# Optimization experiments

Hardware: AMD Instinct MI355X
Metric: run time of the kernel (lower is better)

The kernel has to match this reference:

```python
import jax, jax.numpy as jnp
import numpy as np

N = 50000      # nodes
E = 800000     # edges
H = 8          # heads
D = 16         # per-head dim (hidden_channels)
HD = H * D     # 128
G = 64         # graphs in batch
BN_EPS = 1e-5


def setup_inputs() -> dict:
    key = jax.random.key(0)
    ks = iter(jax.random.split(key, 40))
    s = lambda *shape: jax.random.normal(next(ks), shape, dtype=jnp.float32) * 0.05
    inp = {
        "X": jax.random.normal(next(ks), (N, 1), dtype=jnp.float32),
        "edge_index": jax.random.randint(next(ks), (2, E), 0, N, dtype=jnp.int32),
        "batch": jnp.sort(jax.random.randint(next(ks), (N,), 0, G, dtype=jnp.int32)),
        # layer 1: in=1 -> H*D
        "Wq1": s(1, HD), "bq1": jnp.zeros((HD,), jnp.float32),
        "Wk1": s(1, HD), "bk1": jnp.zeros((HD,), jnp.float32),
        "Wv1": s(1, HD), "bv1": jnp.zeros((HD,), jnp.float32),
        "Ws1": s(1, HD), "bs1": jnp.zeros((HD,), jnp.float32),
        # layers 2-5 stacked: in=HD -> H*D
        "Wq": s(4, HD, HD), "bq": jnp.zeros((4, HD), jnp.float32),
        "Wk": s(4, HD, HD), "bk": jnp.zeros((4, HD), jnp.float32),
        "Wv": s(4, HD, HD), "bv": jnp.zeros((4, HD), jnp.float32),
        "Ws": s(4, HD, HD), "bs": jnp.zeros((4, HD), jnp.float32),
        # batchnorms (5 of them)
        "bn_gamma": jnp.ones((5, HD), jnp.float32),
        "bn_beta": jnp.zeros((5, HD), jnp.float32),
        "Wr": s(HD, 1), "br": jnp.zeros((1,), jnp.float32),
    }
    return inp


def _transformer_conv(x, src, dst, Wq, bq, Wk, bk, Wv, bv, Ws, bs):
    """PyG TransformerConv (concat=True, root_weight=True, beta=False), eval mode."""
    n = x.shape[0]
    q = (x @ Wq + bq).reshape(n, H, D)
    k = (x @ Wk + bk).reshape(n, H, D)
    v = (x @ Wv + bv).reshape(n, H, D)
    # per-edge attention logits: query at destination, key at source
    alpha = jnp.sum(q[dst] * k[src], axis=-1) / jnp.sqrt(jnp.float32(D))  # [E,H]
    # segment softmax over incoming edges of each destination node
    amax = jax.ops.segment_max(alpha, dst, num_segments=n)                # [N,H]
    amax = jnp.where(jnp.isfinite(amax), amax, 0.0)
    ex = jnp.exp(alpha - amax[dst])
    denom = jax.ops.segment_sum(ex, dst, num_segments=n) + 1e-16         # [N,H]
    w = ex / denom[dst]                                                  # [E,H]
    out = jax.ops.segment_sum(v[src] * w[:, :, None], dst, num_segments=n)  # [N,H,D]
    return out.reshape(n, HD) + (x @ Ws + bs)                            # root skip


def _bn(x, gamma, beta):
    mu = jnp.mean(x, axis=0)
    var = jnp.mean(jnp.square(x - mu), axis=0)  # biased, as torch BN training
    return (x - mu) * jax.lax.rsqrt(var + BN_EPS) * gamma + beta


def reference(X, edge_index, batch, Wq1, bq1, Wk1, bk1, Wv1, bv1, Ws1, bs1,
              Wq, bq, Wk, bk, Wv, bv, Ws, bs, bn_gamma, bn_beta, Wr, br):
    src, dst = edge_index[0], edge_index[1]
    x = jax.nn.relu(_transformer_conv(X, src, dst, Wq1, bq1, Wk1, bk1, Wv1, bv1, Ws1, bs1))
    x = _bn(x, bn_gamma[0], bn_beta[0])
    for i in range(4):  # layers 2..5 with residuals (dropout = identity in eval)
        h = jax.nn.relu(_transformer_conv(x, src, dst, Wq[i], bq[i], Wk[i], bk[i],
                                          Wv[i], bv[i], Ws[i], bs[i]))
        x = _bn(h, bn_gamma[i + 1], bn_beta[i + 1]) + x
    # global mean pool over graphs
    sums = jax.ops.segment_sum(x, batch, num_segments=G, indices_are_sorted=True)
    cnts = jax.ops.segment_sum(jnp.ones((x.shape[0],), x.dtype), batch,
                               num_segments=G, indices_are_sorted=True)
    x_mean = sums / jnp.maximum(cnts, 1.0)[:, None]
    pred = x_mean @ Wr + br
    return pred, x_mean
```

## Files before the change

kernel.cpp:

```cpp
#include <hip/hip_runtime.h>
#include <hip/hip_fp16.h>
#include <math.h>

#define HD 128
#define NGRAPH 64

typedef _Float16 f16x8 __attribute__((ext_vector_type(8)));
typedef _Float16 f16x2 __attribute__((ext_vector_type(2)));
typedef float    f32x4 __attribute__((ext_vector_type(4)));

__device__ __forceinline__ unsigned h2bits(__half2 h){ return *(unsigned*)&h; }

__device__ __forceinline__ float fdot2u(unsigned a, unsigned b, float c){
#if __has_builtin(__builtin_amdgcn_fdot2)
  return __builtin_amdgcn_fdot2(*(f16x2*)&a, *(f16x2*)&b, c, false);
#else
  float2 fa = __half22float2(*(__half2*)&a);
  float2 fb = __half22float2(*(__half2*)&b);
  return c + fa.x*fb.x + fa.y*fb.y;
#endif
}

__global__ __launch_bounds__(256) void k_count_setup(
    const int* __restrict__ dst, int* __restrict__ deg, int* __restrict__ epos, int E, int EB,
    const float* __restrict__ X,
    const float* __restrict__ Wq1, const float* __restrict__ bq1,
    const float* __restrict__ Wk1, const float* __restrict__ bk1,
    const float* __restrict__ Wv1, const float* __restrict__ bv1,
    const float* __restrict__ Ws1, const float* __restrict__ bs1,
    const float* __restrict__ Wq, const float* __restrict__ Wk,
    const float* __restrict__ Wv, const float* __restrict__ Ws,
    const int* __restrict__ batch, int* __restrict__ gstart,
    uint4* __restrict__ Wpack,
    unsigned* __restrict__ qh_u, unsigned* __restrict__ kvh_u, unsigned* __restrict__ h_u,
    int N, int L1B){
  int b = blockIdx.x;
  int tid = threadIdx.x;
  if (b < EB){
    int e = b*256 + tid;
    if (e < E) epos[e] = atomicAdd(&deg[dst[e]], 1);
  } else if (b < EB + L1B){
    int idx = (b - EB)*256 + tid;
    if (idx >= N*32) return;
    int n = idx >> 5, s4 = idx & 31, c = s4 << 2;
    float xv = X[n];
    float qv[4], kk[4], vv[4], hv[4];
    #pragma unroll
    for (int i = 0; i < 4; ++i){
      qv[i] = xv*Wq1[c+i] + bq1[c+i];
      kk[i] = xv*Wk1[c+i] + bk1[c+i];
      vv[i] = xv*Wv1[c+i] + bv1[c+i];
      hv[i] = xv*Ws1[c+i] + bs1[c+i];
    }
    uint2 hw;
    hw.x = h2bits(__floats2half2_rn(hv[0], hv[1]));
    hw.y = h2bits(__floats2half2_rn(hv[2], hv[3]));
    *(uint2*)&h_u[(size_t)n*64 + (c >> 1)] = hw;
    uint2 qw;
    qw.x = h2bits(__floats2half2_rn(qv[0], qv[1]));
    qw.y = h2bits(__floats2half2_rn(qv[2], qv[3]));
    *(uint2*)&qh_u[(size_t)n*64 + (c >> 1)] = qw;
    int head = c >> 4, ch = c & 15;
    size_t kbase = (size_t)n*128 + head*16 + (ch >> 1);
    uint2 kw, vw;
    kw.x = h2bits(__floats2half2_rn(kk[0], kk[1]));
    kw.y = h2bits(__floats2half2_rn(kk[2], kk[3]));
    vw.x = h2bits(__floats2half2_rn(vv[0], vv[1]));
    vw.y = h2bits(__floats2half2_rn(vv[2], vv[3]));
    *(uint2*)&kvh_u[kbase]     = kw;
    *(uint2*)&kvh_u[kbase + 8] = vw;
  } else if (b < EB + L1B + 128){
    int idx = (b - EB - L1B)*256 + tid;
    int mi   = idx >> 11;
    int rem  = idx & 2047;
    int lane = rem & 63;
    int tile = rem >> 6;
    int chunk = tile >> 3, nt = tile & 7;
    int l = mi >> 2, ws = mi & 3;
    const float* W = (ws==0?Wq:ws==1?Wk:ws==2?Wv:Ws) + (size_t)l*HD*HD;
    int quad = lane >> 4;
    int n = nt*16 + (lane & 15);
    int k0 = chunk*32 + quad*8;
    __half hs[8];
    #pragma unroll
    for (int j = 0; j < 8; ++j) hs[j] = __float2half(W[(size_t)(k0+j)*HD + n]);
    Wpack[idx] = *(uint4*)hs;
  } else {
    int g = tid;
    if (g > NGRAPH) return;
    int lo = 0, hi = N;
    while (lo < hi){
      int mid = (lo + hi) >> 1;
      if (batch[mid] < g) lo = mid + 1; else hi = mid;
    }
    gstart[g] = lo;
  }
}

__global__ __launch_bounds__(256) void k_scan1(const int* __restrict__ deg, int* __restrict__ rp,
                                               int* __restrict__ bt, int N){
  __shared__ int sm[256];
  int i = blockIdx.x*256 + threadIdx.x;
  int v = (i < N) ? deg[i] : 0;
  sm[threadIdx.x] = v;
  __syncthreads();
  for (int off = 1; off < 256; off <<= 1){
    int t = (threadIdx.x >= (unsigned)off) ? sm[threadIdx.x - off] : 0;
    __syncthreads();
    sm[threadIdx.x] += t;
    __syncthreads();
  }
  if (i < N) rp[i+1] = sm[threadIdx.x];
  if (threadIdx.x == 255) bt[blockIdx.x] = sm[255];
  if (blockIdx.x == 0 && threadIdx.x == 0) rp[0] = 0;
}

__global__ __launch_bounds__(256) void k_scan3(int* __restrict__ rp, const int* __restrict__ bt, int N){
  __shared__ int sm[256];
  int b = blockIdx.x, t = threadIdx.x;
  sm[t] = (t < b) ? bt[t] : 0;
  __syncthreads();
  for (int off = 128; off > 0; off >>= 1){
    if (t < off) sm[t] += sm[t + off];
    __syncthreads();
  }
  int offset = sm[0];
  int i = b*256 + t;
  if (i < N) rp[i+1] += offset;
}

__global__ __launch_bounds__(256) void k_scatter(const int* __restrict__ src, const int* __restrict__ dst,
                                                 const int* __restrict__ rp, const int* __restrict__ epos,
                                                 int* __restrict__ srcs, int E){
  int e = blockIdx.x*256 + threadIdx.x;
  if (e < E) srcs[rp[dst[e]] + epos[e]] = src[e];
}

__global__ __launch_bounds__(256) void k_gemm(
    const __half* __restrict__ x, const uint4* __restrict__ Wpack,
    const float* __restrict__ bq, const float* __restrict__ bk,
    const float* __restrict__ bv, const float* __restrict__ bs,
    unsigned* __restrict__ qh_u, unsigned* __restrict__ kvh_u, unsigned* __restrict__ h_u,
    int N, int layer){
  __shared__ uint4 Bs[2048];
  int wsel = blockIdx.y;
  const uint4* Wm = Wpack + (size_t)(layer*4 + wsel)*2048;
  int tid = threadIdx.x;
  for (int i = tid; i < 2048; i += 256) Bs[i] = Wm[i];

  int w = tid >> 6, lane = tid & 63;
  int l15 = lane & 15, quad = lane >> 4;
  const float* bias = (wsel==0)?bq:(wsel==1)?bk:(wsel==2)?bv:bs;

  __syncthreads();

  for (int rt = 0; rt < 4; ++rt){
    int row0 = blockIdx.x*256 + w*64 + rt*16;
    if (row0 >= N) break;
    int arow = row0 + l15;

    f32x4 acc[8];
    #pragma unroll
    for (int i = 0; i < 8; ++i) acc[i] = (f32x4){0.f,0.f,0.f,0.f};

    #pragma unroll
    for (int chunk = 0; chunk < 4; ++chunk){
      f16x8 a = {};
      if (arow < N) a = *(const f16x8*)(x + (size_t)arow*HD + chunk*32 + quad*8);
      #pragma unroll
      for (int nt = 0; nt < 8; ++nt){
        f16x8 b = *(const f16x8*)&Bs[(chunk*8 + nt)*64 + lane];
        acc[nt] = __builtin_amdgcn_mfma_f32_16x16x32_f16(a, b, acc[nt], 0, 0, 0);
      }
    }

    #pragma unroll
    for (int nt = 0; nt < 8; ++nt){
      int col = nt*16 + l15;
      float b = bias[col];
      #pragma unroll
      for (int reg = 0; reg < 4; ++reg){
        float val = acc[nt][reg] + b;
        float oth = __shfl_xor(val, 1);
        int row = row0 + quad*4 + reg;
        if (!(l15 & 1) && row < N){
          unsigned pk = h2bits(__floats2half2_rn(val, oth));
          if (wsel == 0)       qh_u[(size_t)row*64  + nt*8  + (l15>>1)]      = pk;
          else if (wsel == 1)  kvh_u[(size_t)row*128 + nt*16 + (l15>>1)]     = pk;
          else if (wsel == 2)  kvh_u[(size_t)row*128 + nt*16 + (l15>>1) + 8] = pk;
          else                 h_u[(size_t)row*64  + nt*8  + (l15>>1)]       = pk;
        }
      }
    }
  }
}

__global__ __launch_bounds__(256) void k_attn(
    const uint4* __restrict__ qh4, const uint4* __restrict__ kvh4,
    unsigned* __restrict__ h_u, float* __restrict__ pr2,
    const int* __restrict__ rp, const int* __restrict__ srcs, int N, int layer){
  __shared__ float ssum[4][128];
  __shared__ float ssq[4][128];
  int tid = threadIdx.x;
  int w = tid >> 6, lane = tid & 63;
  int oct = lane >> 3, hh = lane & 7;
  int n = blockIdx.x*4 + w;
  bool active = (n < N);

  float acc[16];
  #pragma unroll
  for (int i = 0; i < 16; ++i) acc[i] = 0.f;
  float lsum = 0.f;

  if (active){
    uint4 q0 = qh4[(size_t)n*16 + hh*2];
    uint4 q1 = qh4[(size_t)n*16 + hh*2 + 1];
    unsigned qr[8] = {q0.x,q0.y,q0.z,q0.w, q1.x,q1.y,q1.z,q1.w};
    int beg = rp[n], end = rp[n+1];
    int t = beg + oct;
    bool vcur = (t < end);
    uint4 g0, g1, g2, g3;
    if (vcur){
      const uint4* base = kvh4 + (size_t)srcs[t]*32 + hh*4;
      g0 = base[0]; g1 = base[1]; g2 = base[2]; g3 = base[3];
    }
    while (vcur){
      int tn = t + 8;
      bool vn = (tn < end);
      int sn = vn ? srcs[tn] : 0;
      const uint4* nb = kvh4 + (size_t)sn*32 + hh*4;
      uint4 n0 = nb[0], n1 = nb[1], n2 = nb[2], n3 = nb[3];

      unsigned kr[8] = {g0.x,g0.y,g0.z,g0.w, g1.x,g1.y,g1.z,g1.w};
      float pd = 0.f;
      #pragma unroll
      for (int i = 0; i < 8; ++i) pd = fdot2u(kr[i], qr[i], pd);
      float e = __expf(pd * 0.25f);
      lsum += e;
      unsigned vr[8] = {g2.x,g2.y,g2.z,g2.w, g3.x,g3.y,g3.z,g3.w};
      #pragma unroll
      for (int i = 0; i < 8; ++i){
        float2 vf = __half22float2(*(__half2*)&vr[i]);
        acc[2*i]   += e*vf.x;
        acc[2*i+1] += e*vf.y;
      }
      g0 = n0; g1 = n1; g2 = n2; g3 = n3;
      t = tn; vcur = vn;
    }
  }

  #pragma unroll
  for (int mask = 8; mask <= 32; mask <<= 1){
    lsum += __shfl_xor(lsum, mask);
    #pragma unroll
    for (int i = 0; i < 16; ++i) acc[i] += __shfl_xor(acc[i], mask);
  }
  float inv = (lsum > 0.f) ? 1.f/lsum : 0.f;

  float out[16];
  #pragma unroll
  for (int i = 0; i < 16; ++i) out[i] = 0.f;
  if (active && oct == 0){
    uint4* hp = (uint4*)(h_u + (size_t)n*64 + hh*8);
    uint4 s0 = hp[0], s1 = hp[1];
    unsigned sr[8] = {s0.x,s0.y,s0.z,s0.w, s1.x,s1.y,s1.z,s1.w};
    #pragma unroll
    for (int i = 0; i < 8; ++i){
      float2 sk = __half22float2(*(__half2*)&sr[i]);
      out[2*i]   = fmaxf(acc[2*i]*inv   + sk.x, 0.f);
      out[2*i+1] = fmaxf(acc[2*i+1]*inv + sk.y, 0.f);
    }
    uint4 w0, w1;
    w0.x = h2bits(__floats2half2_rn(out[0], out[1]));
    w0.y = h2bits(__floats2half2_rn(out[2], out[3]));
    w0.z = h2bits(__floats2half2_rn(out[4], out[5]));
    w0.w = h2bits(__floats2half2_rn(out[6], out[7]));
    w1.x = h2bits(__floats2half2_rn(out[8], out[9]));
    w1.y = h2bits(__floats2half2_rn(out[10], out[11]));
    w1.z = h2bits(__floats2half2_rn(out[12], out[13]));
    w1.w = h2bits(__floats2half2_rn(out[14], out[15]));
    hp[0] = w0; hp[1] = w1;
  }
  if (oct == 0){
    #pragma unroll
    for (int j = 0; j < 16; ++j){
      int pidx = j*8 + hh;
      ssum[w][pidx] = out[j];
      ssq[w][pidx]  = out[j]*out[j];
    }
  }
  __syncthreads();
  float* prow = pr2 + (size_t)(layer & 1)*16384 + (size_t)(blockIdx.x & 63)*256;
  if (tid < 128){
    atomicAdd(&prow[tid], ssum[0][tid]+ssum[1][tid]+ssum[2][tid]+ssum[3][tid]);
  } else {
    int c = tid - 128;
    atomicAdd(&prow[tid], ssq[0][c]+ssq[1][c]+ssq[2][c]+ssq[3][c]);
  }
}

__global__ __launch_bounds__(256) void k_bnfin(
    const uint4* __restrict__ h4, uint4* __restrict__ x4,
    float* __restrict__ pr2, int layer,
    const float* __restrict__ gamma, const float* __restrict__ beta,
    int nchunk, int resid, float invN){
  __shared__ float sscl[128], sbb[128];
  int t = threadIdx.x;
  if (t < 128){
    int c = t;
    int p = ((c & 15) << 3) | (c >> 4);
    const float* pb = pr2 + (size_t)(layer & 1)*16384;
    float s = 0.f, sq = 0.f;
    #pragma unroll 8
    for (int i = 0; i < 64; ++i){
      s  += pb[i*256 + p];
      sq += pb[i*256 + 128 + p];
    }
    float mu  = s * invN;
    float var = sq * invN - mu*mu;
    float scl = rsqrtf(var + 1e-5f) * gamma[c];
    sscl[c] = scl;
    sbb[c]  = beta[c] - mu*scl;
  }
  if (blockIdx.x < 64){
    pr2[(size_t)((layer + 1) & 1)*16384 + (size_t)blockIdx.x*256 + t] = 0.f;
  }
  __syncthreads();
  int stride = gridDim.x * 256;
  for (int ci = blockIdx.x*256 + t; ci < nchunk; ci += stride){
    int cb = (ci & 15) << 3;
    uint4 hv = h4[ci];
    unsigned hr[4] = {hv.x, hv.y, hv.z, hv.w};
    uint4 ov;
    unsigned* op = &ov.x;
    if (resid){
      uint4 xv = x4[ci];
      unsigned xr[4] = {xv.x, xv.y, xv.z, xv.w};
      #pragma unroll
      for (int j = 0; j < 4; ++j){
        float2 hf = __half22float2(*(__half2*)&hr[j]);
        float2 xf = __half22float2(*(__half2*)&xr[j]);
        float o0 = hf.x*sscl[cb+2*j]   + sbb[cb+2*j]   + xf.x;
        float o1 = hf.y*sscl[cb+2*j+1] + sbb[cb+2*j+1] + xf.y;
        op[j] = h2bits(__floats2half2_rn(o0, o1));
      }
    } else {
      #pragma unroll
      for (int j = 0; j < 4; ++j){
        float2 hf = __half22float2(*(__half2*)&hr[j]);
        float o0 = hf.x*sscl[cb+2*j]   + sbb[cb+2*j];
        float o1 = hf.y*sscl[cb+2*j+1] + sbb[cb+2*j+1];
        op[j] = h2bits(__floats2half2_rn(o0, o1));
      }
    }
    x4[ci] = ov;
  }
}

__global__ __launch_bounds__(256) void k_pool1(
    const uint4* __restrict__ x4, const int* __restrict__ gstart,
    float* __restrict__ pp, int N){
  __shared__ float sm[2048];
  int g = blockIdx.x, chunk = blockIdx.y;
  int t = threadIdx.x;
  int tcol = t & 15, trow = t >> 4;
  int start = gstart[g];
  int endr  = gstart[g+1];
  float facc[8];
  #pragma unroll
  for (int j = 0; j < 8; ++j) facc[j] = 0.f;
  for (int r = start + chunk*16 + trow; r < endr; r += 64){
    uint4 v = x4[(size_t)r*16 + tcol];
    unsigned vr[4] = {v.x, v.y, v.z, v.w};
    #pragma unroll
    for (int j = 0; j < 4; ++j){
      float2 f = __half22float2(*(__half2*)&vr[j]);
      facc[2*j]   += f.x;
      facc[2*j+1] += f.y;
    }
  }
  #pragma unroll
  for (int j = 0; j < 8; ++j) sm[t*8 + j] = facc[j];
  __syncthreads();
  if (t < 128){
    float s = 0.f;
    #pragma unroll
    for (int r = 0; r < 16; ++r) s += sm[r*128 + t];
    pp[(size_t)(g*4 + chunk)*128 + t] = s;
  }
}

__global__ __launch_bounds__(128) void k_pool2(
    const float* __restrict__ pp, const int* __restrict__ gstart,
    const float* __restrict__ Wr, const float* __restrict__ br,
    float* __restrict__ out){
  __shared__ float sm[128];
  int g = blockIdx.x, c = threadIdx.x;
  float s = 0.f;
  #pragma unroll
  for (int j = 0; j < 4; ++j) s += pp[(size_t)(g*4 + j)*128 + c];
  int cnt = gstart[g+1] - gstart[g];
  float xm = s / fmaxf((float)cnt, 1.f);
  out[NGRAPH + g*HD + c] = xm;
  sm[c] = xm * Wr[c];
  __syncthreads();
  for (int off = 64; off > 0; off >>= 1){
    if (c < off) sm[c] += sm[c + off];
    __syncthreads();
  }
  if (c == 0) out[g] = sm[0] + br[0];
}

extern "C" void kernel_launch(void* const* d_in, const int* in_sizes, int n_in,
                              void* d_out, int out_size, void* d_ws, size_t ws_size,
                              hipStream_t stream){
  const float* X     = (const float*)d_in[0];
  const int*   ei    = (const int*)  d_in[1];
  const int*   batch = (const int*)  d_in[2];
  const float* Wq1 = (const float*)d_in[3];  const float* bq1 = (const float*)d_in[4];
  const float* Wk1 = (const float*)d_in[5];  const float* bk1 = (const float*)d_in[6];
  const float* Wv1 = (const float*)d_in[7];  const float* bv1 = (const float*)d_in[8];
  const float* Ws1 = (const float*)d_in[9];  const float* bs1 = (const float*)d_in[10];
  const float* Wq  = (const float*)d_in[11]; const float* bq  = (const float*)d_in[12];
  const float* Wk  = (const float*)d_in[13]; const float* bk  = (const float*)d_in[14];
  const float* Wv  = (const float*)d_in[15]; const float* bv  = (const float*)d_in[16];
  const float* Ws  = (const float*)d_in[17]; const float* bs  = (const float*)d_in[18];
  const float* bn_g= (const float*)d_in[19]; const float* bn_b= (const float*)d_in[20];
  const float* Wr  = (const float*)d_in[21]; const float* br  = (const float*)d_in[22];

  const int N = in_sizes[0];
  const int E = in_sizes[1] / 2;

  const int* src = ei;
  const int* dst = ei + E;

  char* p = (char*)d_ws;
  auto alloc = [&](size_t bytes) -> void* {
    void* r = (void*)p;
    p += (bytes + 255) & ~(size_t)255;
    return r;
  };
  int*   deg  = (int*)alloc((size_t)N * 4);
  float* pr2  = (float*)alloc(2 * 64 * 256 * 4);
  char* zero_end = p;
  int* rp     = (int*)alloc((size_t)(N + 1) * 4);
  int* bt     = (int*)alloc(256 * 4);
  int* gstart = (int*)alloc((NGRAPH + 1) * 4);
  int* epos   = (int*)alloc((size_t)E * 4);
  int* srcs   = (int*)alloc((size_t)E * 4);
  float* pp   = (float*)alloc((size_t)NGRAPH * 4 * 128 * 4);
  uint4* Wpack= (uint4*)alloc((size_t)16 * 2048 * 16);
  unsigned* qh_u  = (unsigned*)alloc((size_t)N * 64 * 4);
  unsigned* kvh_u = (unsigned*)alloc((size_t)N * 128 * 4);
  unsigned* h_u   = (unsigned*)alloc((size_t)N * 64 * 4);
  __half* x   = (__half*)alloc((size_t)N * HD * 2);

  hipMemsetAsync(deg, 0, (size_t)(zero_end - (char*)deg), stream);

  const int NB  = (N + 255) / 256;
  const int EB  = (E + 255) / 256;
  const int L1B = (N * 32 + 255) / 256;
  const int NBLK = (N + 3) / 4;
  const int NCH = N * 16;
  const float invN = 1.f / (float)N;

  k_count_setup<<<EB + L1B + 129, 256, 0, stream>>>(
      dst, deg, epos, E, EB,
      X, Wq1,bq1, Wk1,bk1, Wv1,bv1, Ws1,bs1,
      Wq, Wk, Wv, Ws, batch, gstart, Wpack, qh_u, kvh_u, h_u, N, L1B);
  k_scan1  <<<NB, 256, 0, stream>>>(deg, rp, bt, N);
  k_scan3  <<<NB, 256, 0, stream>>>(rp, bt, N);
  k_scatter<<<EB, 256, 0, stream>>>(src, dst, rp, epos, srcs, E);

  k_attn <<<NBLK, 256, 0, stream>>>((const uint4*)qh_u, (const uint4*)kvh_u, h_u, pr2, rp, srcs, N, 0);
  k_bnfin<<<512, 256, 0, stream>>>((const uint4*)h_u, (uint4*)x, pr2, 0, bn_g, bn_b, NCH, 0, invN);

  for (int l = 0; l < 4; ++l){
    k_gemm<<<dim3((N + 255) / 256, 4), 256, 0, stream>>>(
        x, Wpack, bq + (size_t)l*HD, bk + (size_t)l*HD, bv + (size_t)l*HD, bs + (size_t)l*HD,
        qh_u, kvh_u, h_u, N, l);
    k_attn<<<NBLK, 256, 0, stream>>>((const uint4*)qh_u, (const uint4*)kvh_u, h_u, pr2, rp, srcs, N, l + 1);
    k_bnfin<<<512, 256, 0, stream>>>((const uint4*)h_u, (uint4*)x, pr2, l + 1,
                                     bn_g + (size_t)(l+1)*HD, bn_b + (size_t)(l+1)*HD, NCH, 1, invN);
  }

  k_pool1<<<dim3(NGRAPH, 4), 256, 0, stream>>>((const uint4*)x, gstart, pp, N);
  k_pool2<<<NGRAPH, 128, 0, stream>>>(pp, gstart, Wr, br, (float*)d_out);
}
```

Before: 710.0 us.

## Fuse batchnorm finalize and residual into next GEMM prologue and pooling

```diff
diff --git a/kernel.cpp b/kernel.cpp
--- a/kernel.cpp
+++ b/kernel.cpp
@@ -137,17 +137,41 @@
 }
 
 __global__ __launch_bounds__(256) void k_gemm(
-    const __half* __restrict__ x, const uint4* __restrict__ Wpack,
+    const unsigned* __restrict__ hb_in, const unsigned* __restrict__ xold_u,
+    unsigned* __restrict__ xnew_u,
+    const uint4* __restrict__ Wpack,
     const float* __restrict__ bq, const float* __restrict__ bk,
     const float* __restrict__ bv, const float* __restrict__ bs,
-    unsigned* __restrict__ qh_u, unsigned* __restrict__ kvh_u, unsigned* __restrict__ h_u,
-    int N, int layer){
+    unsigned* __restrict__ qh_u, unsigned* __restrict__ kvh_u, unsigned* __restrict__ hskip_u,
+    float* __restrict__ pr2, const float* __restrict__ gamma, const float* __restrict__ beta,
+    int N, int layer, int resid, float invN){
   __shared__ uint4 Bs[2048];
+  __shared__ float sscl[128], sbb[128];
   int wsel = blockIdx.y;
   const uint4* Wm = Wpack + (size_t)(layer*4 + wsel)*2048;
   int tid = threadIdx.x;
   for (int i = tid; i < 2048; i += 256) Bs[i] = Wm[i];
 
+  if (tid < 128){
+    int c = tid;
+    int p = ((c & 15) << 3) | (c >> 4);
+    const float* pb = pr2 + (size_t)(layer & 1)*16384;
+    float s = 0.f, sq = 0.f;
+    #pragma unroll 8
+    for (int i = 0; i < 64; ++i){
+      s  += pb[i*256 + p];
+      sq += pb[i*256 + 128 + p];
+    }
+    float mu  = s * invN;
+    float var = sq * invN - mu*mu;
+    float scl = rsqrtf(var + 1e-5f) * gamma[c];
+    sscl[c] = scl;
+    sbb[c]  = beta[c] - mu*scl;
+  }
+  if (wsel == 0 && blockIdx.x < 64){
+    pr2[(size_t)((layer + 1) & 1)*16384 + (size_t)blockIdx.x*256 + tid] = 0.f;
+  }
+
   int w = tid >> 6, lane = tid & 63;
   int l15 = lane & 15, quad = lane >> 4;
   const float* bias = (wsel==0)?bq:(wsel==1)?bk:(wsel==2)?bv:bs;
@@ -165,12 +189,41 @@
 
     #pragma unroll
     for (int chunk = 0; chunk < 4; ++chunk){
-      f16x8 a = {};
-      if (arow < N) a = *(const f16x8*)(x + (size_t)arow*HD + chunk*32 + quad*8);
+      uint4 au = {0u,0u,0u,0u};
+      if (arow < N){
+        int pbase = chunk*16 + quad*4;
+        int cb = chunk*32 + quad*8;
+        uint4 hv = *(const uint4*)&hb_in[(size_t)arow*64 + pbase];
+        unsigned hr[4] = {hv.x, hv.y, hv.z, hv.w};
+        unsigned ap[4];
+        if (resid){
+          uint4 xv = *(const uint4*)&xold_u[(size_t)arow*64 + pbase];
+          unsigned xr[4] = {xv.x, xv.y, xv.z, xv.w};
+          #pragma unroll
+          for (int j = 0; j < 4; ++j){
+            float2 hf = __half22float2(*(__half2*)&hr[j]);
+            float2 xf = __half22float2(*(__half2*)&xr[j]);
+            float o0 = hf.x*sscl[cb+2*j]   + sbb[cb+2*j]   + xf.x;
+            float o1 = hf.y*sscl[cb+2*j+1] + sbb[cb+2*j+1] + xf.y;
+            ap[j] = h2bits(__floats2half2_rn(o0, o1));
+          }
+        } else {
+          #pragma unroll
+          for (int j = 0; j < 4; ++j){
+            float2 hf = __half22float2(*(__half2*)&hr[j]);
+            float o0 = hf.x*sscl[cb+2*j]   + sbb[cb+2*j];
+            float o1 = hf.y*sscl[cb+2*j+1] + sbb[cb+2*j+1];
+            ap[j] = h2bits(__floats2half2_rn(o0, o1));
+          }
+        }
+        au.x = ap[0]; au.y = ap[1]; au.z = ap[2]; au.w = ap[3];
+        if (wsel == 0) *(uint4*)&xnew_u[(size_t)arow*64 + pbase] = au;
+      }
+      f16x8 a = *(f16x8*)&au;
       #pragma unroll
       for (int nt = 0; nt < 8; ++nt){
-        f16x8 b = *(const f16x8*)&Bs[(chunk*8 + nt)*64 + lane];
-        acc[nt] = __builtin_amdgcn_mfma_f32_16x16x32_f16(a, b, acc[nt], 0, 0, 0);
+        f16x8 bfr = *(const f16x8*)&Bs[(chunk*8 + nt)*64 + lane];
+        acc[nt] = __builtin_amdgcn_mfma_f32_16x16x32_f16(a, bfr, acc[nt], 0, 0, 0);
       }
     }
 
@@ -188,7 +241,7 @@
           if (wsel == 0)       qh_u[(size_t)row*64  + nt*8  + (l15>>1)]      = pk;
           else if (wsel == 1)  kvh_u[(size_t)row*128 + nt*16 + (l15>>1)]     = pk;
           else if (wsel == 2)  kvh_u[(size_t)row*128 + nt*16 + (l15>>1) + 8] = pk;
-          else                 h_u[(size_t)row*64  + nt*8  + (l15>>1)]       = pk;
+          else                 hskip_u[(size_t)row*64 + nt*8 + (l15>>1)]     = pk;
         }
       }
     }
@@ -299,17 +352,17 @@
   }
 }
 
-__global__ __launch_bounds__(256) void k_bnfin(
-    const uint4* __restrict__ h4, uint4* __restrict__ x4,
-    float* __restrict__ pr2, int layer,
-    const float* __restrict__ gamma, const float* __restrict__ beta,
-    int nchunk, int resid, float invN){
+__global__ __launch_bounds__(256) void k_pool1(
+    const uint4* __restrict__ hb4, const uint4* __restrict__ xold4,
+    const int* __restrict__ gstart, float* __restrict__ pp,
+    const float* __restrict__ pb, const float* __restrict__ gamma,
+    const float* __restrict__ beta, float invN){
+  __shared__ float sm[2048];
   __shared__ float sscl[128], sbb[128];
   int t = threadIdx.x;
   if (t < 128){
     int c = t;
     int p = ((c & 15) << 3) | (c >> 4);
-    const float* pb = pr2 + (size_t)(layer & 1)*16384;
     float s = 0.f, sq = 0.f;
     #pragma unroll 8
     for (int i = 0; i < 64; ++i){
@@ -322,61 +375,26 @@
     sscl[c] = scl;
     sbb[c]  = beta[c] - mu*scl;
   }
-  if (blockIdx.x < 64){
-    pr2[(size_t)((layer + 1) & 1)*16384 + (size_t)blockIdx.x*256 + t] = 0.f;
-  }
-  __syncthreads();
-  int stride = gridDim.x * 256;
-  for (int ci = blockIdx.x*256 + t; ci < nchunk; ci += stride){
-    int cb = (ci & 15) << 3;
-    uint4 hv = h4[ci];
-    unsigned hr[4] = {hv.x, hv.y, hv.z, hv.w};
-    uint4 ov;
-    unsigned* op = &ov.x;
-    if (resid){
-      uint4 xv = x4[ci];
-      unsigned xr[4] = {xv.x, xv.y, xv.z, xv.w};
-      #pragma unroll
-      for (int j = 0; j < 4; ++j){
-        float2 hf = __half22float2(*(__half2*)&hr[j]);
-        float2 xf = __half22float2(*(__half2*)&xr[j]);
-        float o0 = hf.x*sscl[cb+2*j]   + sbb[cb+2*j]   + xf.x;
-        float o1 = hf.y*sscl[cb+2*j+1] + sbb[cb+2*j+1] + xf.y;
-        op[j] = h2bits(__floats2half2_rn(o0, o1));
-      }
-    } else {
-      #pragma unroll
-      for (int j = 0; j < 4; ++j){
-        float2 hf = __half22float2(*(__half2*)&hr[j]);
-        float o0 = hf.x*sscl[cb+2*j]   + sbb[cb+2*j];
-        float o1 = hf.y*sscl[cb+2*j+1] + sbb[cb+2*j+1];
-        op[j] = h2bits(__floats2half2_rn(o0, o1));
-      }
-    }
-    x4[ci] = ov;
-  }
-}
-
-__global__ __launch_bounds__(256) void k_pool1(
-    const uint4* __restrict__ x4, const int* __restrict__ gstart,
-    float* __restrict__ pp, int N){
-  __shared__ float sm[2048];
+  __syncthreads();
   int g = blockIdx.x, chunk = blockIdx.y;
-  int t = threadIdx.x;
   int tcol = t & 15, trow = t >> 4;
   int start = gstart[g];
   int endr  = gstart[g+1];
+  int cb = tcol*8;
   float facc[8];
   #pragma unroll
   for (int j = 0; j < 8; ++j) facc[j] = 0.f;
   for (int r = start + chunk*16 + trow; r < endr; r += 64){
-    uint4 v = x4[(size_t)r*16 + tcol];
-    unsigned vr[4] = {v.x, v.y, v.z, v.w};
+    uint4 hv = hb4[(size_t)r*16 + tcol];
+    uint4 xv = xold4[(size_t)r*16 + tcol];
+    unsigned hr[4] = {hv.x, hv.y, hv.z, hv.w};
+    unsigned xr[4] = {xv.x, xv.y, xv.z, xv.w};
     #pragma unroll
     for (int j = 0; j < 4; ++j){
-      float2 f = __half22float2(*(__half2*)&vr[j]);
-      facc[2*j]   += f.x;
-      facc[2*j+1] += f.y;
+      float2 hf = __half22float2(*(__half2*)&hr[j]);
+      float2 xf = __half22float2(*(__half2*)&xr[j]);
+      facc[2*j]   += hf.x*sscl[cb+2*j]   + sbb[cb+2*j]   + xf.x;
+      facc[2*j+1] += hf.y*sscl[cb+2*j+1] + sbb[cb+2*j+1] + xf.y;
     }
   }
   #pragma unroll
@@ -452,8 +470,10 @@
   uint4* Wpack= (uint4*)alloc((size_t)16 * 2048 * 16);
   unsigned* qh_u  = (unsigned*)alloc((size_t)N * 64 * 4);
   unsigned* kvh_u = (unsigned*)alloc((size_t)N * 128 * 4);
-  unsigned* h_u   = (unsigned*)alloc((size_t)N * 64 * 4);
-  __half* x   = (__half*)alloc((size_t)N * HD * 2);
+  unsigned* hb0   = (unsigned*)alloc((size_t)N * 64 * 4);
+  unsigned* hb1   = (unsigned*)alloc((size_t)N * 64 * 4);
+  unsigned* xb0   = (unsigned*)alloc((size_t)N * 64 * 4);
+  unsigned* xb1   = (unsigned*)alloc((size_t)N * 64 * 4);
 
   hipMemsetAsync(deg, 0, (size_t)(zero_end - (char*)deg), stream);
 
@@ -461,29 +481,35 @@
   const int EB  = (E + 255) / 256;
   const int L1B = (N * 32 + 255) / 256;
   const int NBLK = (N + 3) / 4;
-  const int NCH = N * 16;
   const float invN = 1.f / (float)N;
+
+  unsigned* hb[2] = {hb0, hb1};
+  unsigned* xb[2] = {xb0, xb1};
 
   k_count_setup<<<EB + L1B + 129, 256, 0, stream>>>(
       dst, deg, epos, E, EB,
       X, Wq1,bq1, Wk1,bk1, Wv1,bv1, Ws1,bs1,
-      Wq, Wk, Wv, Ws, batch, gstart, Wpack, qh_u, kvh_u, h_u, N, L1B);
+      Wq, Wk, Wv, Ws, batch, gstart, Wpack, qh_u, kvh_u, hb0, N, L1B);
   k_scan1  <<<NB, 256, 0, stream>>>(deg, rp, bt, N);
   k_scan3  <<<NB, 256, 0, stream>>>(rp, bt, N);
   k_scatter<<<EB, 256, 0, stream>>>(src, dst, rp, epos, srcs, E);
 
-  k_attn <<<NBLK, 256, 0, stream>>>((const uint4*)qh_u, (const uint4*)kvh_u, h_u, pr2, rp, srcs, N, 0);
-  k_bnfin<<<512, 256, 0, stream>>>((const uint4*)h_u, (uint4*)x, pr2, 0, bn_g, bn_b, NCH, 0, invN);
+  k_attn<<<NBLK, 256, 0, stream>>>((const uint4*)qh_u, (const uint4*)kvh_u, hb0, pr2, rp, srcs, N, 0);
 
   for (int l = 0; l < 4; ++l){
     k_gemm<<<dim3((N + 255) / 256, 4), 256, 0, stream>>>(
-        x, Wpack, bq + (size_t)l*HD, bk + (size_t)l*HD, bv + (size_t)l*HD, bs + (size_t)l*HD,
-        qh_u, kvh_u, h_u, N, l);
-    k_attn<<<NBLK, 256, 0, stream>>>((const uint4*)qh_u, (const uint4*)kvh_u, h_u, pr2, rp, srcs, N, l + 1);
-    k_bnfin<<<512, 256, 0, stream>>>((const uint4*)h_u, (uint4*)x, pr2, l + 1,
-                                     bn_g + (size_t)(l+1)*HD, bn_b + (size_t)(l+1)*HD, NCH, 1, invN);
-  }
-
-  k_pool1<<<dim3(NGRAPH, 4), 256, 0, stream>>>((const uint4*)x, gstart, pp, N);
+        hb[l & 1], xb[l & 1], xb[(l + 1) & 1],
+        Wpack,
+        bq + (size_t)l*HD, bk + (size_t)l*HD, bv + (size_t)l*HD, bs + (size_t)l*HD,
+        qh_u, kvh_u, hb[(l + 1) & 1],
+        pr2, bn_g + (size_t)l*HD, bn_b + (size_t)l*HD,
+        N, l, (l > 0) ? 1 : 0, invN);
+    k_attn<<<NBLK, 256, 0, stream>>>((const uint4*)qh_u, (const uint4*)kvh_u, hb[(l + 1) & 1],
+                                     pr2, rp, srcs, N, l + 1);
+  }
+
+  k_pool1<<<dim3(NGRAPH, 4), 256, 0, stream>>>(
+      (const uint4*)hb0, (const uint4*)xb0, gstart, pp,
+      pr2 , bn_g + (size_t)4*HD, bn_b + (size_t)4*HD, invN);
   k_pool2<<<NGRAPH, 128, 0, stream>>>(pp, gstart, Wr, br, (float*)d_out);
 }
```

Result: slower. 749.4 us (+5.6%).
